# Performance work log

Hardware: AMD Instinct MI355X
Metric: run time of the kernel (lower is better)

Reference implementation:

```python
import jax, jax.numpy as jnp
import numpy as np

H_SIZE, Z_SIZE, A_SIZE, INTER = 50, 100, 2, 100
T = 16384
SLOPE = 0.01  # torch leaky_relu default


def _lrelu(x):
    return jnp.where(x >= 0, x, SLOPE * x)


def setup_inputs() -> dict:
    key = jax.random.key(0)
    ks = jax.random.split(key, 20)
    s = 0.05
    inp = {
        "z_seq": jax.random.normal(ks[0], (T, 1, Z_SIZE), jnp.float32),
        "a_seq": jax.random.normal(ks[1], (T, 1, A_SIZE), jnp.float32),
        "term_seq": jax.random.uniform(ks[2], (T, 1, 1), jnp.float32),
        "W1": jax.random.normal(ks[3], (100, Z_SIZE + A_SIZE)) * s,
        "b1": jnp.zeros((100,), jnp.float32),
        "W2": jax.random.normal(ks[4], (INTER, 100)) * s,
        "b2": jnp.zeros((INTER,), jnp.float32),
        "W3": jax.random.normal(ks[5], (100, INTER)) * s,
        "b3": jnp.zeros((100,), jnp.float32),
        "W4": jax.random.normal(ks[6], (H_SIZE, 100)) * s,
        "b4": jnp.zeros((H_SIZE,), jnp.float32),
        "W5": jax.random.normal(ks[7], (100, INTER + H_SIZE)) * s,
        "b5": jnp.zeros((100,), jnp.float32),
        "Wz": jax.random.normal(ks[8], (Z_SIZE, 100)) * s,
        "bz": jnp.zeros((Z_SIZE,), jnp.float32),
        "Wt": jax.random.normal(ks[9], (1, 100)) * s,
        "bt": jnp.zeros((1,), jnp.float32),
    }
    return inp


def reference(z_seq, a_seq, term_seq, W1, b1, W2, b2, W3, b3, W4, b4, W5, b5, Wz, bz, Wt, bt):
    def step(h, xs):
        a, z, z_next, term_next = xs  # a:[1,2] z:[1,100] term_next:[1,1]
        # encode_az
        az = jnp.concatenate([a, z], axis=1)  # [1,102]
        inter = _lrelu(az @ W1.T + b1)
        inter = _lrelu(inter @ W2.T + b2)
        # update_h (residual)
        h = h + (_lrelu(inter @ W3.T + b3) @ W4.T + b4)
        # predict_output
        inp = jnp.concatenate([h, inter], axis=1)  # [1,150]
        i5 = _lrelu(inp @ W5.T + b5)
        z_pred = i5 @ Wz.T + bz
        t_logit = i5 @ Wt.T + bt
        z_loss = jnp.mean((z_next - z_pred) ** 2)
        # BCE with logits (stable)
        t_loss = jnp.mean(jnp.maximum(t_logit, 0) - t_logit * term_next
                          + jnp.log1p(jnp.exp(-jnp.abs(t_logit))))
        return h, (z_loss, t_loss)

    h0 = jnp.zeros((1, H_SIZE), z_seq.dtype)
    _, (zl, tl) = jax.lax.scan(
        step, h0, (a_seq[:-1], z_seq[:-1], z_seq[1:], term_seq[1:]))
    z_loss = jnp.mean(zl)
    term_loss = jnp.mean(tl)
    return (z_loss + term_loss, z_loss, term_loss)
```

## Files before the change

### kernel.cpp

```cpp
#include <hip/hip_runtime.h>
#include <hip/hip_bf16.h>
#include <math.h>

#define NS   16383
#define NSP  16384
#define LPB  32
#define NBLK 512
#define TPB  512
#define PACKBLK 80

#define OFF_INTR 0
#define OFF_DELT (OFF_INTR + 1048576)
#define OFF_CSUM (OFF_DELT + 819200)
#define OFF_BZ   (OFF_CSUM + 50*NBLK)
#define OFF_BT   (OFF_BZ + NBLK)
#define OFF_PACK (OFF_BT + NBLK)

#define PK5 57344
#define PKZ 81920
#define PKTOT 98304

using bf16x8 = __attribute__((ext_vector_type(8))) short;
using f32x4  = __attribute__((ext_vector_type(4))) float;

__device__ __forceinline__ unsigned short f2bf(float f) {
    unsigned int x = __float_as_uint(f);
    return (unsigned short)((x + 0x7fffu + ((x >> 16) & 1u)) >> 16);
}
__device__ __forceinline__ float bf2f(unsigned short u) {
    return __uint_as_float(((unsigned int)u) << 16);
}
__device__ __forceinline__ float lrelu(float x) { return fmaxf(x, 0.01f * x); }

__device__ __forceinline__ bf16x8 ldA(const unsigned short* buf, int strideSh, int row, int kc) {
    const int idx = (row * strideSh + kc) ^ ((row & 7) << 3);
    return *(const bf16x8*)(buf + idx);
}
__device__ __forceinline__ bf16x8 ldB(const unsigned short* pk, int KS, int nt, int ks, int lane) {
    return *(const bf16x8*)(pk + (size_t)(((nt * KS + ks) << 6) + lane) * 8);
}
__device__ __forceinline__ bf16x8 loadW(const float* __restrict__ W, const int Kst,
                                        const int klim, const int Nmax,
                                        const int n, const int kbase) {
    const bool nv = (n < Nmax);
    const int nc = nv ? n : (Nmax - 1);
    const float* p = W + (size_t)nc * Kst + kbase;
    float f[8];
    if (kbase + 7 < klim) {
        if ((Kst & 3) == 0) {
            const float4 a = *(const float4*)p;
            const float4 b = *(const float4*)(p + 4);
            f[0]=a.x; f[1]=a.y; f[2]=a.z; f[3]=a.w;
            f[4]=b.x; f[5]=b.y; f[6]=b.z; f[7]=b.w;
        } else {
            #pragma unroll
            for (int q = 0; q < 4; ++q) {
                const float2 t2 = *(const float2*)(p + 2 * q);
                f[2*q] = t2.x; f[2*q+1] = t2.y;
            }
        }
    } else {
        #pragma unroll
        for (int j = 0; j < 8; ++j) f[j] = (kbase + j < klim) ? p[j] : 0.f;
    }
    union { bf16x8 v; unsigned int u[4]; } r;
    #pragma unroll
    for (int q = 0; q < 4; ++q) {
        const float lo = nv ? f[2*q]   : 0.f;
        const float hi = nv ? f[2*q+1] : 0.f;
        const __hip_bfloat162 b2 = __float22bfloat162_rn(make_float2(lo, hi));
        unsigned int uu; __builtin_memcpy(&uu, &b2, 4);
        r.u[q] = uu;
    }
    return r.v;
}
__device__ __forceinline__ f32x4 MF(bf16x8 a, bf16x8 b, f32x4 c) {
    return __builtin_amdgcn_mfma_f32_16x16x32_bf16(a, b, c, 0, 0, 0);
}

#define DLAYER(INBUF, WPTR, KST, KLIM, BIAS, OUTBUF)                            \
    {                                                                           \
        const int nn = w * 16 + rl;                                             \
        const float bv = (nn < 100) ? (BIAS)[nn] : 0.f;                         \
        bf16x8 bfr[4];                                                          \
        _Pragma("unroll")                                                       \
        for (int ks = 0; ks < 4; ++ks)                                          \
            bfr[ks] = loadW(WPTR, KST, KLIM, 100, nn, ks * 32 + g8);            \
        _Pragma("unroll")                                                       \
        for (int m = 0; m < 2; ++m) {                                           \
            f32x4 acc; acc.x = bv; acc.y = bv; acc.z = bv; acc.w = bv;          \
            _Pragma("unroll")                                                   \
            for (int ks = 0; ks < 4; ++ks)                                      \
                acc = MF(ldA(INBUF, 128, m * 16 + rl, ks * 32 + g8), bfr[ks], acc); \
            _Pragma("unroll")                                                   \
            for (int r = 0; r < 4; ++r) {                                       \
                const int row = m * 16 + dr + r;                                \
                (OUTBUF)[((row << 7) + nn) ^ ((row & 7) << 3)] = f2bf(lrelu(acc[r])); \
            }                                                                   \
        }                                                                       \
    }

__global__ __launch_bounds__(TPB, 4)
void k1_encode(const float* __restrict__ z_seq, const float* __restrict__ a_seq,
               const float* __restrict__ W1, const float* __restrict__ b1,
               const float* __restrict__ W2, const float* __restrict__ b2,
               const float* __restrict__ W3, const float* __restrict__ b3,
               const float* __restrict__ W4, const float* __restrict__ b4,
               const float* __restrict__ W5, const float* __restrict__ Wz,
               float* __restrict__ ws)
{
    const int blk = blockIdx.x;
    const int tid = threadIdx.x;

    if (blk >= NBLK) {
        const int idx = PK5 + (blk - NBLK) * TPB + tid;
        int e, KS, layer;
        if (idx < PKZ) { layer = 5; e = idx - PK5; KS = 6; }
        else           { layer = 6; e = idx - PKZ; KS = 4; }
        const int j    = e & 7;
        const int ln   = (e >> 3) & 63;
        const int rest = e >> 9;
        const int ks   = rest % KS;
        const int nt   = rest / KS;
        const int n    = nt * 16 + (ln & 15);
        const int k    = ks * 32 + ((ln >> 4) << 3) + j;
        float v = 0.f;
        if (layer == 5) { if (n < 100) {
                              if (k < 50) v = W5[n * 150 + k];
                              else if (k >= 64 && k < 164) v = W5[n * 150 + k - 14]; } }
        else            { if (n < 100 && k < 100) v = Wz[n * 100 + k]; }
        ((unsigned short*)(ws + OFF_PACK))[idx] = f2bf(v);
        return;
    }

    __shared__ unsigned short Vp[32 * 128];
    __shared__ unsigned short Vq[32 * 128];
    __shared__ float Dl[32 * 64];

    const int lane = tid & 63;
    const int w    = __builtin_amdgcn_readfirstlane(tid >> 6);
    const int t0   = blk * LPB;

    unsigned int* interR = (unsigned int*)(ws + OFF_INTR);
    float* deltaT = ws + OFF_DELT;
    float* csum   = ws + OFF_CSUM;

    if (tid < 32) {
        const int t = tid;
        const float a0 = a_seq[(t0 + t) * 2 + 0];
        const float a1 = a_seq[(t0 + t) * 2 + 1];
        *(unsigned int*)&Vp[((t << 7) + 0) ^ ((t & 7) << 3)] =
            (unsigned int)f2bf(a0) | ((unsigned int)f2bf(a1) << 16);
    }
    for (int i = tid; i < 1600; i += TPB) {
        const int t = i / 50, p = i - t * 50;
        const float2 z2 = *(const float2*)(z_seq + (size_t)(t0 + t) * 100 + 2 * p);
        *(unsigned int*)&Vp[((t << 7) + 2 + 2 * p) ^ ((t & 7) << 3)] =
            (unsigned int)f2bf(z2.x) | ((unsigned int)f2bf(z2.y) << 16);
    }
    for (int i = tid; i < 416; i += TPB) {
        const int t = i / 13, p = i - t * 13;
        *(unsigned int*)&Vp[((t << 7) + 102 + 2 * p) ^ ((t & 7) << 3)] = 0u;
    }
    __syncthreads();

    const int rl = lane & 15;
    const int g8 = (lane >> 4) << 3;
    const int dr = (lane >> 4) << 2;

    DLAYER(Vp, W1, 102, 102, b1, Vq);
    __syncthreads();
    DLAYER(Vq, W2, 100, 100, b2, Vp);
    __syncthreads();
    for (int i = tid; i < 2048; i += TPB) {
        const int t = i >> 6, c2 = i & 63;
        interR[(size_t)(t0 + t) * 64 + c2] =
            *(const unsigned int*)&Vp[((t << 7) + (c2 << 1)) ^ ((t & 7) << 3)];
    }
    DLAYER(Vp, W3, 100, 100, b3, Vq);
    __syncthreads();

    if (w < 4) {
        const int nn = w * 16 + rl;
        const float bv = (nn < 50) ? b4[nn] : 0.f;
        bf16x8 bfr[4];
        #pragma unroll
        for (int ks = 0; ks < 4; ++ks)
            bfr[ks] = loadW(W4, 100, 100, 50, nn, ks * 32 + g8);
        #pragma unroll
        for (int m = 0; m < 2; ++m) {
            f32x4 acc; acc.x = bv; acc.y = bv; acc.z = bv; acc.w = bv;
            #pragma unroll
            for (int ks = 0; ks < 4; ++ks)
                acc = MF(ldA(Vq, 128, m * 16 + rl, ks * 32 + g8), bfr[ks], acc);
            #pragma unroll
            for (int r = 0; r < 4; ++r) {
                const int row = m * 16 + dr + r;
                Dl[row * 64 + (nn ^ row)] = acc[r];
            }
        }
    }
    __syncthreads();

    for (int i = tid; i < 1600; i += TPB) {
        const int n = i >> 5, l = i & 31;
        float v = Dl[l * 64 + (n ^ l)];
        if (t0 + l >= NS) v = 0.f;
        deltaT[n * NSP + t0 + l] = v;
        float s = v;
        #pragma unroll
        for (int off = 16; off > 0; off >>= 1) s += __shfl_xor(s, off, 32);
        if ((lane & 31) == 0) csum[n * NBLK + blk] = s;
    }
}

__global__ __launch_bounds__(TPB, 4)
void k3_predict(const float* __restrict__ z_seq, const float* __restrict__ term_seq,
                const float* __restrict__ b5, const float* __restrict__ bz,
                const float* __restrict__ Wt, const float* __restrict__ bt,
                float* __restrict__ ws)
{
    __shared__ unsigned short Ib[32 * 128];
    __shared__ unsigned short I5[32 * 128];
    __shared__ unsigned short Hb[32 * 64];
    __shared__ float Dl[32 * 64];
    __shared__ float redz[8];

    const int tid  = threadIdx.x;
    const int lane = tid & 63;
    const int w    = __builtin_amdgcn_readfirstlane(tid >> 6);
    const int blk  = blockIdx.x;
    const int t0   = blk * LPB;

    const unsigned short* packw = (const unsigned short*)(ws + OFF_PACK);
    const unsigned int* interR = (const unsigned int*)(ws + OFF_INTR);
    const float* deltaT = ws + OFF_DELT;
    const float* csum   = ws + OFF_CSUM;
    float* g_bz = ws + OFF_BZ;
    float* g_bt = ws + OFF_BT;

    for (int i = tid; i < 2048; i += TPB) {
        const int t = i >> 6, c2 = i & 63;
        *(unsigned int*)&Ib[((t << 7) + (c2 << 1)) ^ ((t & 7) << 3)] =
            interR[(size_t)(t0 + t) * 64 + c2];
    }
    for (int i = tid; i < 1600; i += TPB) {
        const int n = i >> 5, l = i & 31;
        Dl[l * 64 + (n ^ l)] = deltaT[n * NSP + t0 + l];
    }
    for (int i = tid; i < 224; i += TPB) {
        const int t = i / 7, p = i - t * 7;
        *(unsigned int*)&Hb[((t << 6) + 50 + 2 * p) ^ ((t & 7) << 3)] = 0u;
    }
    __syncthreads();

    for (int pass = 0; pass < 4; ++pass) {
        const int n = pass * 16 + w * 2 + (lane >> 5);
        if (n < 50) {
            const int sl = lane & 31;
            float s = 0.f;
            #pragma unroll
            for (int i2 = 0; i2 < 4; ++i2) {
                const int c0 = (sl + (i2 << 5)) << 2;
                if (c0 < blk) {
                    const f32x4 v4 = *(const f32x4*)(csum + n * NBLK + c0);
                    #pragma unroll
                    for (int e = 0; e < 4; ++e)
                        if (c0 + e < blk) s += v4[e];
                }
            }
            #pragma unroll
            for (int off = 16; off > 0; off >>= 1) s += __shfl_xor(s, off, 32);
            float v = Dl[sl * 64 + (n ^ sl)];
            #pragma unroll
            for (int off = 1; off < 32; off <<= 1) {
                const float u = __shfl_up(v, off, 32);
                if (sl >= off) v += u;
            }
            Hb[((sl << 6) + n) ^ ((sl & 7) << 3)] = f2bf(v + s);
        }
    }
    __syncthreads();

    const int rl = lane & 15;
    const int g8 = (lane >> 4) << 3;
    const int dr = (lane >> 4) << 2;

    {
        const int nn = w * 16 + rl;
        const float bv = (nn < 100) ? b5[nn] : 0.f;
        bf16x8 bfr[6];
        #pragma unroll
        for (int ks = 0; ks < 6; ++ks) bfr[ks] = ldB(packw + PK5, 6, w, ks, lane);
        #pragma unroll
        for (int m = 0; m < 2; ++m) {
            f32x4 acc; acc.x = bv; acc.y = bv; acc.z = bv; acc.w = bv;
            #pragma unroll
            for (int ks = 0; ks < 6; ++ks) {
                const bf16x8 a = (ks < 2) ? ldA(Hb, 64, m * 16 + rl, ks * 32 + g8)
                                          : ldA(Ib, 128, m * 16 + rl, (ks - 2) * 32 + g8);
                acc = MF(a, bfr[ks], acc);
            }
            #pragma unroll
            for (int r = 0; r < 4; ++r) {
                const int row = m * 16 + dr + r;
                I5[((row << 7) + nn) ^ ((row & 7) << 3)] = f2bf(lrelu(acc[r]));
            }
        }
    }
    __syncthreads();

    float zpart = 0.f;
    {
        const int nn = w * 16 + rl;
        const float bv = (nn < 100) ? bz[nn] : 0.f;
        bf16x8 bfr[4];
        #pragma unroll
        for (int ks = 0; ks < 4; ++ks) bfr[ks] = ldB(packw + PKZ, 4, w, ks, lane);
        #pragma unroll
        for (int m = 0; m < 2; ++m) {
            f32x4 acc; acc.x = bv; acc.y = bv; acc.z = bv; acc.w = bv;
            #pragma unroll
            for (int ks = 0; ks < 4; ++ks)
                acc = MF(ldA(I5, 128, m * 16 + rl, ks * 32 + g8), bfr[ks], acc);
            if (nn < 100) {
                #pragma unroll
                for (int r = 0; r < 4; ++r) {
                    const int row = m * 16 + dr + r;
                    if (t0 + row < NS) {
                        const float zn = z_seq[(size_t)(t0 + row + 1) * 100 + nn];
                        const float d = zn - acc[r];
                        zpart += d * d;
                    }
                }
            }
        }
    }

    float tpart = 0.f;
    if (w == 0 && lane < 32) {
        const bool vl = (t0 + lane) < NS;
        float a = bt[0];
        #pragma unroll
        for (int g = 0; g < 13; ++g) {
            const bf16x8 v = *(const bf16x8*)(I5 + (((lane << 7) + 8 * g) ^ ((lane & 7) << 3)));
            #pragma unroll
            for (int j = 0; j < 8; ++j) {
                const int c = 8 * g + j;
                if (c < 100) a = fmaf(bf2f((unsigned short)v[j]), Wt[c], a);
            }
        }
        if (vl) {
            const float y = term_seq[t0 + lane + 1];
            tpart = fmaxf(a, 0.f) - a * y + log1pf(expf(-fabsf(a)));
        }
    }

    #pragma unroll
    for (int off = 32; off > 0; off >>= 1) zpart += __shfl_xor(zpart, off, 64);
    if (lane == 0) redz[w] = zpart;
    __syncthreads();
    if (tid == 0) {
        float s = 0.f;
        #pragma unroll
        for (int i = 0; i < 8; ++i) s += redz[i];
        g_bz[blk] = s;
    }
    if (w == 0) {
        #pragma unroll
        for (int off = 16; off > 0; off >>= 1) tpart += __shfl_xor(tpart, off, 32);
        if (lane == 0) g_bt[blk] = tpart;
    }
}

__global__ __launch_bounds__(512)
void k4_final(const float* __restrict__ ws, float* __restrict__ out)
{
    __shared__ float rz[8], rt[8];
    const float* g_bz = ws + OFF_BZ;
    const float* g_bt = ws + OFF_BT;
    const int tid  = threadIdx.x;
    const int lane = tid & 63;
    const int w    = tid >> 6;
    float z = g_bz[tid];
    float t = g_bt[tid];
    #pragma unroll
    for (int off = 32; off > 0; off >>= 1) {
        z += __shfl_xor(z, off, 64);
        t += __shfl_xor(t, off, 64);
    }
    if (lane == 0) { rz[w] = z; rt[w] = t; }
    __syncthreads();
    if (tid == 0) {
        float sz = 0.f, st = 0.f;
        #pragma unroll
        for (int i = 0; i < 8; ++i) { sz += rz[i]; st += rt[i]; }
        const float zl = sz / (100.0f * NS);
        const float tl = st / NS;
        out[0] = zl + tl;
        out[1] = zl;
        out[2] = tl;
    }
}

extern "C" void kernel_launch(void* const* d_in, const int* in_sizes, int n_in,
                              void* d_out, int out_size, void* d_ws, size_t ws_size,
                              hipStream_t stream)
{
    const float* z_seq = (const float*)d_in[0];
    const float* a_seq = (const float*)d_in[1];
    const float* term  = (const float*)d_in[2];
    const float* W1 = (const float*)d_in[3];  const float* b1 = (const float*)d_in[4];
    const float* W2 = (const float*)d_in[5];  const float* b2 = (const float*)d_in[6];
    const float* W3 = (const float*)d_in[7];  const float* b3 = (const float*)d_in[8];
    const float* W4 = (const float*)d_in[9];  const float* b4 = (const float*)d_in[10];
    const float* W5 = (const float*)d_in[11]; const float* b5 = (const float*)d_in[12];
    const float* Wz = (const float*)d_in[13]; const float* bz = (const float*)d_in[14];
    const float* Wt = (const float*)d_in[15]; const float* bt = (const float*)d_in[16];
    float* out = (float*)d_out;
    float* ws  = (float*)d_ws;

    k1_encode<<<NBLK + PACKBLK, TPB, 0, stream>>>(z_seq, a_seq, W1, b1, W2, b2,
                                                  W3, b3, W4, b4, W5, Wz, ws);
    k3_predict<<<NBLK, TPB, 0, stream>>>(z_seq, term, b5, bz, Wt, bt, ws);
    k4_final<<<1, 512, 0, stream>>>(ws, out);
}
```

Before: 32.66 us.

## Fuse encode, predict and final reduction into one kernel with decoupled look-back scan

Merges the three kernels into a single launch. A ticket counter assigns virtual block IDs, and a decoupled look-back scan propagates the per-block h-delta sums across blocks, so the hidden state prefix no longer needs a global csum pass. Intermediate activations stay in shared memory instead of round-tripping through the workspace. W5 and Wz are now loaded directly from fp32 rather than from a prepacked bf16 buffer. Final losses are combined with atomics plus a last-block-done counter, which requires a memset launch and adds spin-waiting between blocks.

```diff
diff --git a/kernel.cpp b/kernel.cpp
--- a/kernel.cpp
+++ b/kernel.cpp
@@ -3,22 +3,12 @@
 #include <math.h>
 
 #define NS   16383
-#define NSP  16384
 #define LPB  32
 #define NBLK 512
 #define TPB  512
-#define PACKBLK 80
-
-#define OFF_INTR 0
-#define OFF_DELT (OFF_INTR + 1048576)
-#define OFF_CSUM (OFF_DELT + 819200)
-#define OFF_BZ   (OFF_CSUM + 50*NBLK)
-#define OFF_BT   (OFF_BZ + NBLK)
-#define OFF_PACK (OFF_BT + NBLK)
-
-#define PK5 57344
-#define PKZ 81920
-#define PKTOT 98304
+
+#define WSB_ST 64
+#define WS_ZERO_BYTES (64 + (size_t)NBLK * 64 * 8)
 
 using bf16x8 = __attribute__((ext_vector_type(8))) short;
 using f32x4  = __attribute__((ext_vector_type(4))) float;
@@ -35,9 +25,6 @@
 __device__ __forceinline__ bf16x8 ldA(const unsigned short* buf, int strideSh, int row, int kc) {
     const int idx = (row * strideSh + kc) ^ ((row & 7) << 3);
     return *(const bf16x8*)(buf + idx);
-}
-__device__ __forceinline__ bf16x8 ldB(const unsigned short* pk, int KS, int nt, int ks, int lane) {
-    return *(const bf16x8*)(pk + (size_t)(((nt * KS + ks) << 6) + lane) * 8);
 }
 __device__ __forceinline__ bf16x8 loadW(const float* __restrict__ W, const int Kst,
                                         const int klim, const int Nmax,
@@ -101,49 +88,44 @@
     }
 
 __global__ __launch_bounds__(TPB, 4)
-void k1_encode(const float* __restrict__ z_seq, const float* __restrict__ a_seq,
-               const float* __restrict__ W1, const float* __restrict__ b1,
-               const float* __restrict__ W2, const float* __restrict__ b2,
-               const float* __restrict__ W3, const float* __restrict__ b3,
-               const float* __restrict__ W4, const float* __restrict__ b4,
-               const float* __restrict__ W5, const float* __restrict__ Wz,
-               float* __restrict__ ws)
+void fused(const float* __restrict__ z_seq, const float* __restrict__ a_seq,
+           const float* __restrict__ term_seq,
+           const float* __restrict__ W1, const float* __restrict__ b1,
+           const float* __restrict__ W2, const float* __restrict__ b2,
+           const float* __restrict__ W3, const float* __restrict__ b3,
+           const float* __restrict__ W4, const float* __restrict__ b4,
+           const float* __restrict__ W5, const float* __restrict__ b5,
+           const float* __restrict__ Wz, const float* __restrict__ bz,
+           const float* __restrict__ Wt, const float* __restrict__ bt,
+           float* __restrict__ ws, float* __restrict__ out)
 {
-    const int blk = blockIdx.x;
-    const int tid = threadIdx.x;
-
-    if (blk >= NBLK) {
-        const int idx = PK5 + (blk - NBLK) * TPB + tid;
-        int e, KS, layer;
-        if (idx < PKZ) { layer = 5; e = idx - PK5; KS = 6; }
-        else           { layer = 6; e = idx - PKZ; KS = 4; }
-        const int j    = e & 7;
-        const int ln   = (e >> 3) & 63;
-        const int rest = e >> 9;
-        const int ks   = rest % KS;
-        const int nt   = rest / KS;
-        const int n    = nt * 16 + (ln & 15);
-        const int k    = ks * 32 + ((ln >> 4) << 3) + j;
-        float v = 0.f;
-        if (layer == 5) { if (n < 100) {
-                              if (k < 50) v = W5[n * 150 + k];
-                              else if (k >= 64 && k < 164) v = W5[n * 150 + k - 14]; } }
-        else            { if (n < 100 && k < 100) v = Wz[n * 100 + k]; }
-        ((unsigned short*)(ws + OFF_PACK))[idx] = f2bf(v);
-        return;
-    }
-
     __shared__ unsigned short Vp[32 * 128];
     __shared__ unsigned short Vq[32 * 128];
+    __shared__ unsigned short Hb[32 * 64];
     __shared__ float Dl[32 * 64];
-
+    __shared__ float csum_s[64];
+    __shared__ float coff_s[64];
+    __shared__ float redz[8];
+    __shared__ unsigned int vid_s;
+
+    const int tid  = threadIdx.x;
     const int lane = tid & 63;
     const int w    = __builtin_amdgcn_readfirstlane(tid >> 6);
-    const int t0   = blk * LPB;
-
-    unsigned int* interR = (unsigned int*)(ws + OFF_INTR);
-    float* deltaT = ws + OFF_DELT;
-    float* csum   = ws + OFF_CSUM;
+
+    unsigned int* ticket = (unsigned int*)ws;
+    unsigned int* done   = (unsigned int*)ws + 1;
+    float* accz = ws + 2;
+    float* acct = ws + 3;
+    unsigned long long* st = (unsigned long long*)((char*)ws + WSB_ST);
+
+    if (tid == 0) vid_s = atomicAdd(ticket, 1u);
+    for (int i = tid; i < 224; i += TPB) {
+        const int t = i / 7, p = i - t * 7;
+        *(unsigned int*)&Hb[((t << 6) + 50 + 2 * p) ^ ((t & 7) << 3)] = 0u;
+    }
+    __syncthreads();
+    const int vid = __builtin_amdgcn_readfirstlane((int)vid_s);
+    const int t0  = vid * LPB;
 
     if (tid < 32) {
         const int t = tid;
@@ -172,11 +154,6 @@
     __syncthreads();
     DLAYER(Vq, W2, 100, 100, b2, Vp);
     __syncthreads();
-    for (int i = tid; i < 2048; i += TPB) {
-        const int t = i >> 6, c2 = i & 63;
-        interR[(size_t)(t0 + t) * 64 + c2] =
-            *(const unsigned int*)&Vp[((t << 7) + (c2 << 1)) ^ ((t & 7) << 3)];
-    }
     DLAYER(Vp, W3, 100, 100, b3, Vq);
     __syncthreads();
 
@@ -205,52 +182,93 @@
     for (int i = tid; i < 1600; i += TPB) {
         const int n = i >> 5, l = i & 31;
         float v = Dl[l * 64 + (n ^ l)];
-        if (t0 + l >= NS) v = 0.f;
-        deltaT[n * NSP + t0 + l] = v;
+        if (t0 + l >= NS) { v = 0.f; Dl[l * 64 + (n ^ l)] = 0.f; }
         float s = v;
         #pragma unroll
         for (int off = 16; off > 0; off >>= 1) s += __shfl_xor(s, off, 32);
-        if ((lane & 31) == 0) csum[n * NBLK + blk] = s;
-    }
-}
-
-__global__ __launch_bounds__(TPB, 4)
-void k3_predict(const float* __restrict__ z_seq, const float* __restrict__ term_seq,
-                const float* __restrict__ b5, const float* __restrict__ bz,
-                const float* __restrict__ Wt, const float* __restrict__ bt,
-                float* __restrict__ ws)
-{
-    __shared__ unsigned short Ib[32 * 128];
-    __shared__ unsigned short I5[32 * 128];
-    __shared__ unsigned short Hb[32 * 64];
-    __shared__ float Dl[32 * 64];
-    __shared__ float redz[8];
-
-    const int tid  = threadIdx.x;
-    const int lane = tid & 63;
-    const int w    = __builtin_amdgcn_readfirstlane(tid >> 6);
-    const int blk  = blockIdx.x;
-    const int t0   = blk * LPB;
-
-    const unsigned short* packw = (const unsigned short*)(ws + OFF_PACK);
-    const unsigned int* interR = (const unsigned int*)(ws + OFF_INTR);
-    const float* deltaT = ws + OFF_DELT;
-    const float* csum   = ws + OFF_CSUM;
-    float* g_bz = ws + OFF_BZ;
-    float* g_bt = ws + OFF_BT;
-
-    for (int i = tid; i < 2048; i += TPB) {
-        const int t = i >> 6, c2 = i & 63;
-        *(unsigned int*)&Ib[((t << 7) + (c2 << 1)) ^ ((t & 7) << 3)] =
-            interR[(size_t)(t0 + t) * 64 + c2];
-    }
-    for (int i = tid; i < 1600; i += TPB) {
-        const int n = i >> 5, l = i & 31;
-        Dl[l * 64 + (n ^ l)] = deltaT[n * NSP + t0 + l];
-    }
-    for (int i = tid; i < 224; i += TPB) {
-        const int t = i / 7, p = i - t * 7;
-        *(unsigned int*)&Hb[((t << 6) + 50 + 2 * p) ^ ((t & 7) << 3)] = 0u;
+        if ((lane & 31) == 0) {
+            csum_s[n] = s;
+            const unsigned long long pk =
+                ((unsigned long long)(vid == 0 ? 2u : 1u) << 32) |
+                (unsigned long long)__float_as_uint(s);
+            __hip_atomic_store(&st[(size_t)vid * 64 + n], pk,
+                               __ATOMIC_RELAXED, __HIP_MEMORY_SCOPE_AGENT);
+        }
+    }
+    __syncthreads();
+
+    {
+        float pref0=0.f,pref1=0.f,pref2=0.f,pref3=0.f,pref4=0.f,pref5=0.f,pref6=0.f;
+        int   base0=vid-1,base1=vid-1,base2=vid-1,base3=vid-1,base4=vid-1,base5=vid-1,base6=vid-1;
+        unsigned int alive = 0;
+        #pragma unroll
+        for (int j = 0; j < 7; ++j)
+            if (w + 8 * j < 50 && vid > 0) alive |= (1u << j);
+
+        #define LB_LOAD(J, BASE, SV)                                            \
+            unsigned long long SV = 0ull;                                       \
+            if (alive & (1u << J)) {                                            \
+                const int p = (BASE) - lane;                                    \
+                if (p >= 0)                                                     \
+                    SV = __hip_atomic_load(&st[(size_t)p * 64 + (w + 8 * J)],   \
+                             __ATOMIC_RELAXED, __HIP_MEMORY_SCOPE_AGENT);       \
+            }
+        #define LB_PROC(J, BASE, PREF, SV)                                      \
+            if (alive & (1u << J)) {                                            \
+                const int p = (BASE) - lane;                                    \
+                const unsigned int tag = (unsigned int)(SV >> 32);              \
+                const bool isIncl  = (p < 0) || (tag == 2u);                    \
+                const bool isValid = (p < 0) || (tag != 0u);                    \
+                if (!(~__ballot(isValid))) {                                    \
+                    const unsigned long long im = __ballot(isIncl);             \
+                    if (im) {                                                   \
+                        const int fl = (int)__ffsll((long long)im) - 1;         \
+                        float c = (lane <= fl && p >= 0)                        \
+                                  ? __uint_as_float((unsigned int)SV) : 0.f;    \
+                        _Pragma("unroll")                                       \
+                        for (int o = 32; o > 0; o >>= 1) c += __shfl_xor(c, o, 64); \
+                        PREF += c;                                              \
+                        alive &= ~(1u << J);                                    \
+                    } else {                                                    \
+                        float c = __uint_as_float((unsigned int)SV);            \
+                        _Pragma("unroll")                                       \
+                        for (int o = 32; o > 0; o >>= 1) c += __shfl_xor(c, o, 64); \
+                        PREF += c;                                              \
+                        BASE -= 64;                                             \
+                    }                                                           \
+                }                                                               \
+            }
+
+        while (alive) {
+            LB_LOAD(0, base0, sv0) LB_LOAD(1, base1, sv1) LB_LOAD(2, base2, sv2)
+            LB_LOAD(3, base3, sv3) LB_LOAD(4, base4, sv4) LB_LOAD(5, base5, sv5)
+            LB_LOAD(6, base6, sv6)
+            LB_PROC(0, base0, pref0, sv0) LB_PROC(1, base1, pref1, sv1)
+            LB_PROC(2, base2, pref2, sv2) LB_PROC(3, base3, pref3, sv3)
+            LB_PROC(4, base4, pref4, sv4) LB_PROC(5, base5, pref5, sv5)
+            LB_PROC(6, base6, pref6, sv6)
+        }
+        #undef LB_LOAD
+        #undef LB_PROC
+
+        if (lane == 0) {
+            #define LB_FIN(J, PREF)                                             \
+                {                                                               \
+                    const int n = w + 8 * J;                                    \
+                    if (n < 50) {                                               \
+                        coff_s[n] = PREF;                                       \
+                        if (vid > 0) {                                          \
+                            const unsigned long long pk = (2ull << 32) |        \
+                                (unsigned long long)__float_as_uint(PREF + csum_s[n]); \
+                            __hip_atomic_store(&st[(size_t)vid * 64 + n], pk,   \
+                                __ATOMIC_RELAXED, __HIP_MEMORY_SCOPE_AGENT);    \
+                        } else coff_s[n] = 0.f;                                 \
+                    }                                                           \
+                }
+            LB_FIN(0, pref0) LB_FIN(1, pref1) LB_FIN(2, pref2) LB_FIN(3, pref3)
+            LB_FIN(4, pref4) LB_FIN(5, pref5) LB_FIN(6, pref6)
+            #undef LB_FIN
+        }
     }
     __syncthreads();
 
@@ -258,53 +276,39 @@
         const int n = pass * 16 + w * 2 + (lane >> 5);
         if (n < 50) {
             const int sl = lane & 31;
-            float s = 0.f;
-            #pragma unroll
-            for (int i2 = 0; i2 < 4; ++i2) {
-                const int c0 = (sl + (i2 << 5)) << 2;
-                if (c0 < blk) {
-                    const f32x4 v4 = *(const f32x4*)(csum + n * NBLK + c0);
-                    #pragma unroll
-                    for (int e = 0; e < 4; ++e)
-                        if (c0 + e < blk) s += v4[e];
-                }
-            }
-            #pragma unroll
-            for (int off = 16; off > 0; off >>= 1) s += __shfl_xor(s, off, 32);
             float v = Dl[sl * 64 + (n ^ sl)];
             #pragma unroll
             for (int off = 1; off < 32; off <<= 1) {
                 const float u = __shfl_up(v, off, 32);
                 if (sl >= off) v += u;
             }
-            Hb[((sl << 6) + n) ^ ((sl & 7) << 3)] = f2bf(v + s);
-        }
-    }
-    __syncthreads();
-
-    const int rl = lane & 15;
-    const int g8 = (lane >> 4) << 3;
-    const int dr = (lane >> 4) << 2;
+            Hb[((sl << 6) + n) ^ ((sl & 7) << 3)] = f2bf(v + coff_s[n]);
+        }
+    }
+    __syncthreads();
 
     {
         const int nn = w * 16 + rl;
         const float bv = (nn < 100) ? b5[nn] : 0.f;
         bf16x8 bfr[6];
-        #pragma unroll
-        for (int ks = 0; ks < 6; ++ks) bfr[ks] = ldB(packw + PK5, 6, w, ks, lane);
+        bfr[0] = loadW(W5, 150, 50, 100, nn, g8);
+        bfr[1] = loadW(W5, 150, 50, 100, nn, 32 + g8);
+        #pragma unroll
+        for (int ks = 2; ks < 6; ++ks)
+            bfr[ks] = loadW(W5, 150, 150, 100, nn, ks * 32 + g8 - 14);
         #pragma unroll
         for (int m = 0; m < 2; ++m) {
             f32x4 acc; acc.x = bv; acc.y = bv; acc.z = bv; acc.w = bv;
             #pragma unroll
             for (int ks = 0; ks < 6; ++ks) {
                 const bf16x8 a = (ks < 2) ? ldA(Hb, 64, m * 16 + rl, ks * 32 + g8)
-                                          : ldA(Ib, 128, m * 16 + rl, (ks - 2) * 32 + g8);
+                                          : ldA(Vp, 128, m * 16 + rl, (ks - 2) * 32 + g8);
                 acc = MF(a, bfr[ks], acc);
             }
             #pragma unroll
             for (int r = 0; r < 4; ++r) {
                 const int row = m * 16 + dr + r;
-                I5[((row << 7) + nn) ^ ((row & 7) << 3)] = f2bf(lrelu(acc[r]));
+                Vq[((row << 7) + nn) ^ ((row & 7) << 3)] = f2bf(lrelu(acc[r]));
             }
         }
     }
@@ -316,13 +320,14 @@
         const float bv = (nn < 100) ? bz[nn] : 0.f;
         bf16x8 bfr[4];
         #pragma unroll
-        for (int ks = 0; ks < 4; ++ks) bfr[ks] = ldB(packw + PKZ, 4, w, ks, lane);
+        for (int ks = 0; ks < 4; ++ks)
+            bfr[ks] = loadW(Wz, 100, 100, 100, nn, ks * 32 + g8);
         #pragma unroll
         for (int m = 0; m < 2; ++m) {
             f32x4 acc; acc.x = bv; acc.y = bv; acc.z = bv; acc.w = bv;
             #pragma unroll
             for (int ks = 0; ks < 4; ++ks)
-                acc = MF(ldA(I5, 128, m * 16 + rl, ks * 32 + g8), bfr[ks], acc);
+                acc = MF(ldA(Vq, 128, m * 16 + rl, ks * 32 + g8), bfr[ks], acc);
             if (nn < 100) {
                 #pragma unroll
                 for (int r = 0; r < 4; ++r) {
@@ -343,7 +348,7 @@
         float a = bt[0];
         #pragma unroll
         for (int g = 0; g < 13; ++g) {
-            const bf16x8 v = *(const bf16x8*)(I5 + (((lane << 7) + 8 * g) ^ ((lane & 7) << 3)));
+            const bf16x8 v = *(const bf16x8*)(Vq + (((lane << 7) + 8 * g) ^ ((lane & 7) << 3)));
             #pragma unroll
             for (int j = 0; j < 8; ++j) {
                 const int c = 8 * g + j;
@@ -359,47 +364,28 @@
     #pragma unroll
     for (int off = 32; off > 0; off >>= 1) zpart += __shfl_xor(zpart, off, 64);
     if (lane == 0) redz[w] = zpart;
+    if (w == 0) {
+        #pragma unroll
+        for (int off = 16; off > 0; off >>= 1) tpart += __shfl_xor(tpart, off, 32);
+    }
     __syncthreads();
     if (tid == 0) {
         float s = 0.f;
         #pragma unroll
         for (int i = 0; i < 8; ++i) s += redz[i];
-        g_bz[blk] = s;
-    }
-    if (w == 0) {
-        #pragma unroll
-        for (int off = 16; off > 0; off >>= 1) tpart += __shfl_xor(tpart, off, 32);
-        if (lane == 0) g_bt[blk] = tpart;
-    }
-}
-
-__global__ __launch_bounds__(512)
-void k4_final(const float* __restrict__ ws, float* __restrict__ out)
-{
-    __shared__ float rz[8], rt[8];
-    const float* g_bz = ws + OFF_BZ;
-    const float* g_bt = ws + OFF_BT;
-    const int tid  = threadIdx.x;
-    const int lane = tid & 63;
-    const int w    = tid >> 6;
-    float z = g_bz[tid];
-    float t = g_bt[tid];
-    #pragma unroll
-    for (int off = 32; off > 0; off >>= 1) {
-        z += __shfl_xor(z, off, 64);
-        t += __shfl_xor(t, off, 64);
-    }
-    if (lane == 0) { rz[w] = z; rt[w] = t; }
-    __syncthreads();
-    if (tid == 0) {
-        float sz = 0.f, st = 0.f;
-        #pragma unroll
-        for (int i = 0; i < 8; ++i) { sz += rz[i]; st += rt[i]; }
-        const float zl = sz / (100.0f * NS);
-        const float tl = st / NS;
-        out[0] = zl + tl;
-        out[1] = zl;
-        out[2] = tl;
+        atomicAdd(accz, s);
+        atomicAdd(acct, tpart);
+        const unsigned int old =
+            __hip_atomic_fetch_add(done, 1u, __ATOMIC_ACQ_REL, __HIP_MEMORY_SCOPE_AGENT);
+        if (old == (unsigned int)(NBLK - 1)) {
+            const float sz  = __hip_atomic_load(accz, __ATOMIC_RELAXED, __HIP_MEMORY_SCOPE_AGENT);
+            const float stt = __hip_atomic_load(acct, __ATOMIC_RELAXED, __HIP_MEMORY_SCOPE_AGENT);
+            const float zl = sz / (100.0f * NS);
+            const float tl = stt / NS;
+            out[0] = zl + tl;
+            out[1] = zl;
+            out[2] = tl;
+        }
     }
 }
 
@@ -420,8 +406,8 @@
     float* out = (float*)d_out;
     float* ws  = (float*)d_ws;
 
-    k1_encode<<<NBLK + PACKBLK, TPB, 0, stream>>>(z_seq, a_seq, W1, b1, W2, b2,
-                                                  W3, b3, W4, b4, W5, Wz, ws);
-    k3_predict<<<NBLK, TPB, 0, stream>>>(z_seq, term, b5, bz, Wt, bt, ws);
-    k4_final<<<1, 512, 0, stream>>>(ws, out);
-}
+    hipMemsetAsync(ws, 0, WS_ZERO_BYTES, stream);
+    fused<<<NBLK, TPB, 0, stream>>>(z_seq, a_seq, term,
+                                    W1, b1, W2, b2, W3, b3, W4, b4,
+                                    W5, b5, Wz, bz, Wt, bt, ws, out);
+}
```

Result: slower. 111.4 us (+241.1%).
